# Optimization experiments

Hardware: AMD Instinct MI355X
Metric: run time of the kernel (lower is better)

## Reference

```python
import jax, jax.numpy as jnp
import numpy as np

EPS = 1e-12  # matches torch F.normalize default eps

def l2norm(t):
    n = jnp.linalg.norm(t, axis=-1, keepdims=True)
    return t / jnp.maximum(n, EPS)

def rotate_half(x):
    # '... (j d) -> ... j d' with j=2: split into two halves, return cat(-x2, x1)
    x1, x2 = jnp.split(x, 2, axis=-1)
    return jnp.concatenate((-x2, x1), axis=-1)

def rotary_freqs(seq_len, dim):
    inv_freq = 1.0 / (10000.0 ** (jnp.arange(0, dim, 2, dtype=jnp.float32) / dim))
    seq = jnp.arange(seq_len, dtype=jnp.float32)
    freqs = seq[:, None] * inv_freq[None, :]          # [n, d/2]
    emb = jnp.concatenate((freqs, freqs), axis=-1)    # [n, d]
    return emb[None, None]                            # [1, 1, n, d]

def apply_rotary_pos_emb(t, freqs):
    # rot_dim == dim_head here, so the pass-through slice is empty
    return t * jnp.cos(freqs) + rotate_half(t) * jnp.sin(freqs)

def setup_inputs() -> dict:
    key = jax.random.key(0)
    kq, kk, kv = jax.random.split(key, 3)
    b, h, n, d = 2, 16, 2048, 64
    q = jax.random.normal(kq, (b, h, n, d), dtype=jnp.float32)
    k = jax.random.normal(kk, (b, h, n, d), dtype=jnp.float32)
    v = jax.random.normal(kv, (b, h, n, d), dtype=jnp.float32)
    q_scale = jnp.ones((d,), dtype=jnp.float32)
    k_scale = jnp.ones((d,), dtype=jnp.float32)
    return {"q": q, "k": k, "v": v, "q_scale": q_scale, "k_scale": k_scale}

def reference(q, k, v, q_scale, k_scale):
    b, h, n, d = q.shape
    # QK RMSNorm (l2 normalize + learned per-dim scale)
    q = l2norm(q) * q_scale
    k = l2norm(k) * k_scale
    # rotary position embedding (always applied in the source module)
    freqs = rotary_freqs(n, d)
    q = apply_rotary_pos_emb(q, freqs)
    k = apply_rotary_pos_emb(k, freqs)
    # attention: explicit scores -> softmax -> values
    scale = d ** -0.5
    sim = jnp.einsum('bhid,bhjd->bhij', q, k) * scale
    attn = jax.nn.softmax(sim, axis=-1)
    out = jnp.einsum('bhij,bhjd->bhid', attn, v)
    # 'b h n d -> b n (h d)'
    return out.transpose(0, 2, 1, 3).reshape(b, n, h * d)
```

## Files before the change

### kernel.cpp

```cpp
#include <hip/hip_runtime.h>
#include <math.h>

#define BH   32
#define NSEQ 2048
#define DH   64
#define NH   16
#define LOG2E 1.44269504088896f

typedef _Float16 f16x8 __attribute__((ext_vector_type(8)));
typedef __fp16   fp16x2 __attribute__((ext_vector_type(2)));
typedef float    f32x16v __attribute__((ext_vector_type(16)));
typedef unsigned uint2v __attribute__((ext_vector_type(2)));

#if __has_builtin(__builtin_amdgcn_exp2f)
#define EXP2F(x) __builtin_amdgcn_exp2f(x)
#else
#define EXP2F(x) exp2f(x)
#endif

static __device__ __forceinline__ unsigned pkrtz(float a, float b) {
    fp16x2 r = __builtin_amdgcn_cvt_pkrtz(a, b);
    return __builtin_bit_cast(unsigned, r);
}
static __device__ __forceinline__ unsigned packh_rne(float a, float b) {
    union { _Float16 h[2]; unsigned u; } x;
    x.h[0] = (_Float16)a; x.h[1] = (_Float16)b;
    return x.u;
}

static __device__ __forceinline__ float2 rope_cs(int pos, int p) {
    float invf_rev = EXP2F(-(float)p * (13.287712379549449f / 32.0f)) * 0.15915494309189535f;
    float rev = (float)pos * invf_rev;
    float fr = rev - floorf(rev);
    float th = fr * 6.283185307179586f;
    return make_float2(__cosf(th), __sinf(th));
}

__global__ __launch_bounds__(256) void prep_all(
    const float* __restrict__ q, const float* __restrict__ k, const float* __restrict__ v,
    const float* __restrict__ qs, const float* __restrict__ ksc,
    unsigned* __restrict__ qh, unsigned* __restrict__ kh, unsigned* __restrict__ vt2) {
    const int bid = blockIdx.x;
    const int t = threadIdx.x;
    if (bid < 16384) {
        const bool isq = bid < 8192;
        const float* in = isq ? q : k;
        const float* sc = isq ? qs : ksc;
        const float smul = isq ? 0.125f * LOG2E : 1.0f;
        const int sb = bid & 8191;
        const int w = t >> 6, lane = t & 63;
        const int c = lane & 31, hfr = lane >> 5;
        const int row = sb * 8 + w * 2 + hfr;
        float2 x2 = *(const float2*)(in + (size_t)row * DH + 2 * c);
        float ss = x2.x * x2.x + x2.y * x2.y;
        #pragma unroll
        for (int off = 16; off > 0; off >>= 1) ss += __shfl_xor(ss, off);
        float inv = 1.0f / fmaxf(sqrtf(ss), 1e-12f);
        float2 s2 = *(const float2*)(sc + 2 * c);
        float t0 = x2.x * inv * s2.x;
        float t1 = x2.y * inv * s2.y;
        float p0 = __shfl_xor(t0, 16);
        float p1 = __shfl_xor(t1, 16);
        float r0 = (c < 16) ? -p0 : p0;
        float r1 = (c < 16) ? -p1 : p1;
        int pos = row & (NSEQ - 1);
        int pp = (2 * c) & 31;
        float2 cs0 = rope_cs(pos, pp);
        float2 cs1 = rope_cs(pos, pp + 1);
        float o0 = (t0 * cs0.x + r0 * cs0.y) * smul;
        float o1 = (t1 * cs1.x + r1 * cs1.y) * smul;
        unsigned val = packh_rne(o0, o1);
        if (isq) {
            qh[row * 32 + c] = val;
        } else {
            const int rloc = row & (NSEQ - 1);
            const unsigned idx = (unsigned)((rloc >> 5) * 1024 + (c >> 3) * 256
                               + ((c >> 2) & 1) * 128 + (rloc & 31) * 4 + (c & 3));
            kh[(size_t)(row >> 11) * 65536 + idx] = val;
        }
    } else {
        const int sb = bid - 16384;
        const int kt = sb & 31, bh = sb >> 5;
        __shared__ float Lv[64 * 68];
        #pragma unroll
        for (int i = 0; i < 4; ++i) {
            int chunk = t + 256 * i;
            int r = chunk >> 4, fg = chunk & 15;
            *(float4*)&Lv[r * 68 + fg * 4] =
                *(const float4*)(v + ((size_t)bh * NSEQ + kt * 64 + r) * DH + fg * 4);
        }
        __syncthreads();
        const int d = t & 63, kg = t >> 6;
        unsigned u[8];
        #pragma unroll
        for (int j = 0; j < 8; ++j) {
            int ky = kg * 16 + 2 * j;
            u[j] = pkrtz(Lv[ky * 68 + d], Lv[(ky + 1) * 68 + d]);
        }
        const int rh = d >> 5, cc = d & 31;
        unsigned* dst = vt2 + (size_t)bh * 65536
                      + (size_t)((kt * 4 + kg) * 2 + rh) * 256 + cc * 4;
        *(uint4*)(dst)       = make_uint4(u[0], u[1], u[2], u[3]);
        *(uint4*)(dst + 128) = make_uint4(u[4], u[5], u[6], u[7]);
    }
}

static __device__ __forceinline__ f16x8 ld8(const unsigned* p) {
    return *(const f16x8*)p;
}

static __device__ __forceinline__ void attn_step(
    const f16x8 (&kc)[4], const f16x8 (&vc)[4],
    f16x8 (&kn)[4], f16x8 (&vn)[4],
    const unsigned* kp, const unsigned* vp, bool pre,
    const f16x8 (&qf)[4], f32x16v (&o)[2], float& lpart, int hf)
{
    if (pre) {
        #pragma unroll
        for (int ks = 0; ks < 4; ++ks) kn[ks] = ld8(kp + ks * 256);
        #pragma unroll
        for (int kk = 0; kk < 2; ++kk)
            #pragma unroll
            for (int rh = 0; rh < 2; ++rh)
                vn[kk * 2 + rh] = ld8(vp + kk * 512 + rh * 256);
    }
    f32x16v s;
    #pragma unroll
    for (int r = 0; r < 16; ++r) s[r] = 0.f;
    #pragma unroll
    for (int ks = 0; ks < 4; ++ks)
        s = __builtin_amdgcn_mfma_f32_32x32x16_f16(kc[ks], qf[ks], s, 0, 0, 0);
    #pragma unroll
    for (int r = 0; r < 16; ++r) {
        float pv = EXP2F(s[r]);
        s[r] = pv;
        lpart += pv;
    }
    #pragma unroll
    for (int kk = 0; kk < 2; ++kk) {
        unsigned P01 = pkrtz(s[kk * 8 + 0], s[kk * 8 + 1]);
        unsigned P23 = pkrtz(s[kk * 8 + 2], s[kk * 8 + 3]);
        unsigned P45 = pkrtz(s[kk * 8 + 4], s[kk * 8 + 5]);
        unsigned P67 = pkrtz(s[kk * 8 + 6], s[kk * 8 + 7]);
        union { unsigned u[4]; f16x8 v; } B;
#if __has_builtin(__builtin_amdgcn_permlane32_swap)
        uint2v r02 = __builtin_amdgcn_permlane32_swap(P01, P45, 0, 0);
        uint2v r13 = __builtin_amdgcn_permlane32_swap(P23, P67, 0, 0);
        B.u[0] = r02[0]; B.u[1] = r13[0]; B.u[2] = r02[1]; B.u[3] = r13[1];
#else
        unsigned x01 = (unsigned)__shfl_xor((int)P01, 32);
        unsigned x23 = (unsigned)__shfl_xor((int)P23, 32);
        unsigned x45 = (unsigned)__shfl_xor((int)P45, 32);
        unsigned x67 = (unsigned)__shfl_xor((int)P67, 32);
        B.u[0] = hf ? x45 : P01;
        B.u[1] = hf ? x67 : P23;
        B.u[2] = hf ? P45 : x01;
        B.u[3] = hf ? P67 : x23;
#endif
        o[0] = __builtin_amdgcn_mfma_f32_32x32x16_f16(vc[kk * 2 + 0], B.v, o[0], 0, 0, 0);
        o[1] = __builtin_amdgcn_mfma_f32_32x32x16_f16(vc[kk * 2 + 1], B.v, o[1], 0, 0, 0);
    }
}

__global__ __launch_bounds__(256, 3) void attn_kernel(
    const unsigned* __restrict__ qh, const unsigned* __restrict__ kf,
    const unsigned* __restrict__ vf, float* __restrict__ out) {

    __shared__ float Lred[128 * 33];

    const int flat = (blockIdx.x & 7) * 128 + (blockIdx.x >> 3);
    const int bh = flat >> 5, qb = flat & 31;

    const int tid = threadIdx.x;
    const int w = tid >> 6, lane = tid & 63;
    const int c = lane & 31, hf = lane >> 5;
    const int qhw = w & 1;
    const int khw = w >> 1;

    const _Float16* qbase = (const _Float16*)qh + ((size_t)bh * NSEQ + qb * 64) * DH;
    f16x8 qf[4];
    #pragma unroll
    for (int ks = 0; ks < 4; ++ks)
        qf[ks] = *(const f16x8*)(qbase + (qhw * 32 + c) * DH + ks * 16 + hf * 8);

    const unsigned* kfb = kf + (size_t)bh * 65536 + khw * 1024 + lane * 4;
    const unsigned* vfb = vf + (size_t)bh * 65536 + khw * 1024 + lane * 4;

    f16x8 ka[4], va[4], kb[4], vb[4];
    #pragma unroll
    for (int ks = 0; ks < 4; ++ks) ka[ks] = ld8(kfb + ks * 256);
    #pragma unroll
    for (int kk = 0; kk < 2; ++kk)
        #pragma unroll
        for (int rh = 0; rh < 2; ++rh)
            va[kk * 2 + rh] = ld8(vfb + kk * 512 + rh * 256);

    f32x16v o[2];
    #pragma unroll
    for (int mt = 0; mt < 2; ++mt)
        #pragma unroll
        for (int r = 0; r < 16; ++r) o[mt][r] = 0.f;
    float lpart = 0.f;

    for (int jt = 0; jt < 32; jt += 2) {
        attn_step(ka, va, kb, vb,
                  kfb + (size_t)(jt + 1) * 2048, vfb + (size_t)(jt + 1) * 2048,
                  true, qf, o, lpart, hf);
        attn_step(kb, vb, ka, va,
                  kfb + (size_t)(jt + 2) * 2048, vfb + (size_t)(jt + 2) * 2048,
                  jt + 2 < 32, qf, o, lpart, hf);
    }

    float lw = lpart + __shfl_xor(lpart, 32);
    if (w >= 2) {
        const int base = ((w - 2) * 64 + lane) * 33;
        #pragma unroll
        for (int mt = 0; mt < 2; ++mt)
            #pragma unroll
            for (int r = 0; r < 16; ++r) Lred[base + mt * 16 + r] = o[mt][r];
        Lred[base + 32] = lw;
    }
    __syncthreads();
    if (w < 2) {
        const int base = (w * 64 + lane) * 33;
        #pragma unroll
        for (int mt = 0; mt < 2; ++mt)
            #pragma unroll
            for (int r = 0; r < 16; ++r) o[mt][r] += Lred[base + mt * 16 + r];
        lw += Lred[base + 32];
        float invl = 1.0f / lw;
        const int b = bh >> 4, h = bh & 15;
        const int pos = qb * 64 + w * 32 + c;
        float* obase = out + ((size_t)b * NSEQ + pos) * (NH * DH) + h * DH;
        #pragma unroll
        for (int mt = 0; mt < 2; ++mt)
            #pragma unroll
            for (int g = 0; g < 4; ++g) {
                float4 r4 = make_float4(o[mt][g * 4 + 0] * invl, o[mt][g * 4 + 1] * invl,
                                        o[mt][g * 4 + 2] * invl, o[mt][g * 4 + 3] * invl);
                *(float4*)(obase + mt * 32 + g * 8 + hf * 4) = r4;
            }
    }
}

extern "C" void kernel_launch(void* const* d_in, const int* in_sizes, int n_in,
                              void* d_out, int out_size, void* d_ws, size_t ws_size,
                              hipStream_t stream) {
    const float* q  = (const float*)d_in[0];
    const float* k  = (const float*)d_in[1];
    const float* v  = (const float*)d_in[2];
    const float* qs = (const float*)d_in[3];
    const float* ks = (const float*)d_in[4];
    float* outp = (float*)d_out;

    unsigned* qh  = (unsigned*)d_ws;
    unsigned* kh  = qh + (size_t)BH * NSEQ * 32;
    unsigned* vt2 = kh + (size_t)BH * NSEQ * 32;

    prep_all<<<17408, 256, 0, stream>>>(q, k, v, qs, ks, qh, kh, vt2);
    attn_kernel<<<1024, 256, 0, stream>>>(qh, kh, vt2, outp);
}
```

Before: 144.6 us.

## Process two query tiles per block to reuse K/V fragments across tiles

Each block now handles 128 query rows as two 64-row tiles that share every loaded K and V fragment, so K/V global traffic per query drops by half and the grid shrinks to 512 blocks. Launch bounds drop to 2 blocks per CU to make room for the doubled accumulators. The row-sum of probabilities is now accumulated with fdot2 on the packed fp16 values rather than scalar fp32 adds, which slightly changes rounding. The cost is higher register pressure, lower occupancy and fewer blocks to spread across CUs.

After: 143.6 us. About the same (-0.7%).

```diff
diff --git a/kernel.cpp b/kernel.cpp
--- a/kernel.cpp
+++ b/kernel.cpp
@@ -9,6 +9,7 @@
 
 typedef _Float16 f16x8 __attribute__((ext_vector_type(8)));
 typedef __fp16   fp16x2 __attribute__((ext_vector_type(2)));
+typedef _Float16 half2v __attribute__((ext_vector_type(2)));
 typedef float    f32x16v __attribute__((ext_vector_type(16)));
 typedef unsigned uint2v __attribute__((ext_vector_type(2)));
 
@@ -109,39 +110,27 @@
     return *(const f16x8*)p;
 }
 
-static __device__ __forceinline__ void attn_step(
-    const f16x8 (&kc)[4], const f16x8 (&vc)[4],
-    f16x8 (&kn)[4], f16x8 (&vn)[4],
-    const unsigned* kp, const unsigned* vp, bool pre,
-    const f16x8 (&qf)[4], f32x16v (&o)[2], float& lpart, int hf)
+static __device__ __forceinline__ void pv_tile(
+    f32x16v& s, const f16x8 (&vc)[4], f32x16v (&ot)[2], float& lp, int hf)
 {
-    if (pre) {
-        #pragma unroll
-        for (int ks = 0; ks < 4; ++ks) kn[ks] = ld8(kp + ks * 256);
-        #pragma unroll
-        for (int kk = 0; kk < 2; ++kk)
-            #pragma unroll
-            for (int rh = 0; rh < 2; ++rh)
-                vn[kk * 2 + rh] = ld8(vp + kk * 512 + rh * 256);
-    }
-    f32x16v s;
-    #pragma unroll
-    for (int r = 0; r < 16; ++r) s[r] = 0.f;
-    #pragma unroll
-    for (int ks = 0; ks < 4; ++ks)
-        s = __builtin_amdgcn_mfma_f32_32x32x16_f16(kc[ks], qf[ks], s, 0, 0, 0);
-    #pragma unroll
-    for (int r = 0; r < 16; ++r) {
-        float pv = EXP2F(s[r]);
-        s[r] = pv;
-        lpart += pv;
-    }
+    #pragma unroll
+    for (int r = 0; r < 16; ++r) s[r] = EXP2F(s[r]);
     #pragma unroll
     for (int kk = 0; kk < 2; ++kk) {
         unsigned P01 = pkrtz(s[kk * 8 + 0], s[kk * 8 + 1]);
         unsigned P23 = pkrtz(s[kk * 8 + 2], s[kk * 8 + 3]);
         unsigned P45 = pkrtz(s[kk * 8 + 4], s[kk * 8 + 5]);
         unsigned P67 = pkrtz(s[kk * 8 + 6], s[kk * 8 + 7]);
+#if __has_builtin(__builtin_amdgcn_fdot2)
+        const half2v one2 = {(_Float16)1.0f, (_Float16)1.0f};
+        lp = __builtin_amdgcn_fdot2(__builtin_bit_cast(half2v, P01), one2, lp, false);
+        lp = __builtin_amdgcn_fdot2(__builtin_bit_cast(half2v, P23), one2, lp, false);
+        lp = __builtin_amdgcn_fdot2(__builtin_bit_cast(half2v, P45), one2, lp, false);
+        lp = __builtin_amdgcn_fdot2(__builtin_bit_cast(half2v, P67), one2, lp, false);
+#else
+        #pragma unroll
+        for (int r = 0; r < 8; ++r) lp += s[kk * 8 + r];
+#endif
         union { unsigned u[4]; f16x8 v; } B;
 #if __has_builtin(__builtin_amdgcn_permlane32_swap)
         uint2v r02 = __builtin_amdgcn_permlane32_swap(P01, P45, 0, 0);
@@ -157,19 +146,46 @@
         B.u[2] = hf ? P45 : x01;
         B.u[3] = hf ? P67 : x23;
 #endif
-        o[0] = __builtin_amdgcn_mfma_f32_32x32x16_f16(vc[kk * 2 + 0], B.v, o[0], 0, 0, 0);
-        o[1] = __builtin_amdgcn_mfma_f32_32x32x16_f16(vc[kk * 2 + 1], B.v, o[1], 0, 0, 0);
-    }
-}
-
-__global__ __launch_bounds__(256, 3) void attn_kernel(
+        ot[0] = __builtin_amdgcn_mfma_f32_32x32x16_f16(vc[kk * 2 + 0], B.v, ot[0], 0, 0, 0);
+        ot[1] = __builtin_amdgcn_mfma_f32_32x32x16_f16(vc[kk * 2 + 1], B.v, ot[1], 0, 0, 0);
+    }
+}
+
+static __device__ __forceinline__ void attn_step(
+    const f16x8 (&kc)[4], const f16x8 (&vc)[4],
+    f16x8 (&kn)[4], f16x8 (&vn)[4],
+    const unsigned* kp, const unsigned* vp, bool pre,
+    const f16x8 (&qf)[2][4], f32x16v (&o)[2][2], float (&lp)[2],
+    const f32x16v& z16, int hf)
+{
+    if (pre) {
+        #pragma unroll
+        for (int ks = 0; ks < 4; ++ks) kn[ks] = ld8(kp + ks * 256);
+        #pragma unroll
+        for (int kk = 0; kk < 2; ++kk)
+            #pragma unroll
+            for (int rh = 0; rh < 2; ++rh)
+                vn[kk * 2 + rh] = ld8(vp + kk * 512 + rh * 256);
+    }
+    f32x16v s0 = __builtin_amdgcn_mfma_f32_32x32x16_f16(kc[0], qf[0][0], z16, 0, 0, 0);
+    f32x16v s1 = __builtin_amdgcn_mfma_f32_32x32x16_f16(kc[0], qf[1][0], z16, 0, 0, 0);
+    #pragma unroll
+    for (int ks = 1; ks < 4; ++ks) {
+        s0 = __builtin_amdgcn_mfma_f32_32x32x16_f16(kc[ks], qf[0][ks], s0, 0, 0, 0);
+        s1 = __builtin_amdgcn_mfma_f32_32x32x16_f16(kc[ks], qf[1][ks], s1, 0, 0, 0);
+    }
+    pv_tile(s0, vc, o[0], lp[0], hf);
+    pv_tile(s1, vc, o[1], lp[1], hf);
+}
+
+__global__ __launch_bounds__(256, 2) void attn_kernel(
     const unsigned* __restrict__ qh, const unsigned* __restrict__ kf,
     const unsigned* __restrict__ vf, float* __restrict__ out) {
 
     __shared__ float Lred[128 * 33];
 
-    const int flat = (blockIdx.x & 7) * 128 + (blockIdx.x >> 3);
-    const int bh = flat >> 5, qb = flat & 31;
+    const int flat = (blockIdx.x & 7) * 64 + (blockIdx.x >> 3);
+    const int bh = flat >> 4, qb = flat & 15;
 
     const int tid = threadIdx.x;
     const int w = tid >> 6, lane = tid & 63;
@@ -177,11 +193,13 @@
     const int qhw = w & 1;
     const int khw = w >> 1;
 
-    const _Float16* qbase = (const _Float16*)qh + ((size_t)bh * NSEQ + qb * 64) * DH;
-    f16x8 qf[4];
-    #pragma unroll
-    for (int ks = 0; ks < 4; ++ks)
-        qf[ks] = *(const f16x8*)(qbase + (qhw * 32 + c) * DH + ks * 16 + hf * 8);
+    const _Float16* qbase = (const _Float16*)qh + ((size_t)bh * NSEQ + qb * 128) * DH;
+    f16x8 qf[2][4];
+    #pragma unroll
+    for (int t = 0; t < 2; ++t)
+        #pragma unroll
+        for (int ks = 0; ks < 4; ++ks)
+            qf[t][ks] = *(const f16x8*)(qbase + (t * 64 + qhw * 32 + c) * DH + ks * 16 + hf * 8);
 
     const unsigned* kfb = kf + (size_t)bh * 65536 + khw * 1024 + lane * 4;
     const unsigned* vfb = vf + (size_t)bh * 65536 + khw * 1024 + lane * 4;
@@ -195,51 +213,63 @@
         for (int rh = 0; rh < 2; ++rh)
             va[kk * 2 + rh] = ld8(vfb + kk * 512 + rh * 256);
 
-    f32x16v o[2];
-    #pragma unroll
-    for (int mt = 0; mt < 2; ++mt)
-        #pragma unroll
-        for (int r = 0; r < 16; ++r) o[mt][r] = 0.f;
-    float lpart = 0.f;
+    f32x16v z16;
+    #pragma unroll
+    for (int r = 0; r < 16; ++r) z16[r] = 0.f;
+
+    f32x16v o[2][2];
+    #pragma unroll
+    for (int t = 0; t < 2; ++t)
+        #pragma unroll
+        for (int mt = 0; mt < 2; ++mt)
+            #pragma unroll
+            for (int r = 0; r < 16; ++r) o[t][mt][r] = 0.f;
+    float lp[2] = {0.f, 0.f};
 
     for (int jt = 0; jt < 32; jt += 2) {
         attn_step(ka, va, kb, vb,
                   kfb + (size_t)(jt + 1) * 2048, vfb + (size_t)(jt + 1) * 2048,
-                  true, qf, o, lpart, hf);
+                  true, qf, o, lp, z16, hf);
         attn_step(kb, vb, ka, va,
                   kfb + (size_t)(jt + 2) * 2048, vfb + (size_t)(jt + 2) * 2048,
-                  jt + 2 < 32, qf, o, lpart, hf);
-    }
-
-    float lw = lpart + __shfl_xor(lpart, 32);
-    if (w >= 2) {
-        const int base = ((w - 2) * 64 + lane) * 33;
-        #pragma unroll
-        for (int mt = 0; mt < 2; ++mt)
-            #pragma unroll
-            for (int r = 0; r < 16; ++r) Lred[base + mt * 16 + r] = o[mt][r];
-        Lred[base + 32] = lw;
-    }
-    __syncthreads();
-    if (w < 2) {
-        const int base = (w * 64 + lane) * 33;
-        #pragma unroll
-        for (int mt = 0; mt < 2; ++mt)
-            #pragma unroll
-            for (int r = 0; r < 16; ++r) o[mt][r] += Lred[base + mt * 16 + r];
-        lw += Lred[base + 32];
-        float invl = 1.0f / lw;
-        const int b = bh >> 4, h = bh & 15;
-        const int pos = qb * 64 + w * 32 + c;
-        float* obase = out + ((size_t)b * NSEQ + pos) * (NH * DH) + h * DH;
-        #pragma unroll
-        for (int mt = 0; mt < 2; ++mt)
-            #pragma unroll
-            for (int g = 0; g < 4; ++g) {
-                float4 r4 = make_float4(o[mt][g * 4 + 0] * invl, o[mt][g * 4 + 1] * invl,
-                                        o[mt][g * 4 + 2] * invl, o[mt][g * 4 + 3] * invl);
-                *(float4*)(obase + mt * 32 + g * 8 + hf * 4) = r4;
-            }
+                  jt + 2 < 32, qf, o, lp, z16, hf);
+    }
+
+    float lw[2];
+    #pragma unroll
+    for (int t = 0; t < 2; ++t) lw[t] = lp[t] + __shfl_xor(lp[t], 32);
+
+    const int b = bh >> 4, h = bh & 15;
+    #pragma unroll
+    for (int t = 0; t < 2; ++t) {
+        if (t) __syncthreads();
+        if (w >= 2) {
+            const int base = ((w - 2) * 64 + lane) * 33;
+            #pragma unroll
+            for (int mt = 0; mt < 2; ++mt)
+                #pragma unroll
+                for (int r = 0; r < 16; ++r) Lred[base + mt * 16 + r] = o[t][mt][r];
+            Lred[base + 32] = lw[t];
+        }
+        __syncthreads();
+        if (w < 2) {
+            const int base = (w * 64 + lane) * 33;
+            #pragma unroll
+            for (int mt = 0; mt < 2; ++mt)
+                #pragma unroll
+                for (int r = 0; r < 16; ++r) o[t][mt][r] += Lred[base + mt * 16 + r];
+            float invl = 1.0f / (lw[t] + Lred[base + 32]);
+            const int pos = qb * 128 + t * 64 + w * 32 + c;
+            float* obase = out + ((size_t)b * NSEQ + pos) * (NH * DH) + h * DH;
+            #pragma unroll
+            for (int mt = 0; mt < 2; ++mt)
+                #pragma unroll
+                for (int g = 0; g < 4; ++g) {
+                    float4 r4 = make_float4(o[t][mt][g * 4 + 0] * invl, o[t][mt][g * 4 + 1] * invl,
+                                            o[t][mt][g * 4 + 2] * invl, o[t][mt][g * 4 + 3] * invl);
+                    *(float4*)(obase + mt * 32 + g * 8 + hf * 4) = r4;
+                }
+        }
     }
 }
 
@@ -258,5 +288,5 @@
     unsigned* vt2 = kh + (size_t)BH * NSEQ * 32;
 
     prep_all<<<17408, 256, 0, stream>>>(q, k, v, qs, ks, qh, kh, vt2);
-    attn_kernel<<<1024, 256, 0, stream>>>(qh, kh, vt2, outp);
-}
+    attn_kernel<<<512, 256, 0, stream>>>(qh, kh, vt2, outp);
+}
```
